# Kernel optimization log

Hardware: AMD Instinct MI355X
Metric: run time of the kernel (lower is better)

Reference implementation:

```python
import jax, jax.numpy as jnp
import numpy as np

ALPHA = 0.2  # LeakyReLU negative slope
NEG_INF = -9e15

def leaky_relu(x):
    return jnp.where(x >= 0, x, ALPHA * x)

def setup_inputs() -> dict:
    key = jax.random.key(0)
    ks = jax.random.split(key, 7)
    B, N, D = 8, 1024, 256
    R = 12
    return {
        "h0": jax.random.normal(ks[0], (B, N, D), jnp.float32),
        "h1": jax.random.normal(ks[1], (B, N, D), jnp.float32),
        "multi_adj": jax.random.randint(ks[2], (R, B, N, N), 0, 2, jnp.int32),
        "adj": jax.random.randint(ks[3], (B, N, N), 0, 2, jnp.int32),
        "W": jax.random.normal(ks[4], (D, D), jnp.float32) * 0.05,
        "a": jax.random.normal(ks[5], (2 * D,), jnp.float32) * 0.05,
        "A_rel": jax.random.normal(ks[6], (R, 2 * D), jnp.float32) * 0.05,
    }

def reference(h0, h1, multi_adj, adj, W, a, A_rel):
    D = W.shape[1]
    Wh0 = jnp.einsum('bnd,de->bne', h0, W)  # [B,N0,D]
    Wh1 = jnp.einsum('bnd,de->bne', h1, W)  # [B,N1,D]
    # a_input @ v decomposes into outer-sum of per-node projections
    s0 = Wh0 @ a[:D]                         # [B,N0]
    s1 = Wh1 @ a[D:]                         # [B,N1]
    e = leaky_relu(s0[:, :, None] + s1[:, None, :])  # [B,N0,N1]
    attention = jnp.where(adj > 0, e, NEG_INF)
    # 12 relation score maps, fused: r0[r,b,i] + r1[r,b,j]
    r0 = jnp.einsum('bnd,rd->rbn', Wh0, A_rel[:, :D])  # [R,B,N0]
    r1 = jnp.einsum('bnd,rd->rbn', Wh1, A_rel[:, D:])  # [R,B,N1]
    e_rel = leaky_relu(r0[:, :, :, None] + r1[:, :, None, :])  # [R,B,N0,N1]
    rel_sum = jnp.where(multi_adj > 0, e_rel, 0.0).sum(axis=0)  # [B,N0,N1]
    # note: original softmax is over dim=1 (source-node axis N0)
    att = jax.nn.softmax(attention + 0.01 * rel_sum, axis=1)
    # dropout omitted (eval mode / deterministic baseline)
    h_prime = jnp.einsum('bij,bjd->bid', att, Wh1)
    return jax.nn.elu(h_prime)  # concat=True
```

## Files before the change

### kernel.cpp

```cpp
#include <hip/hip_runtime.h>
#include <hip/hip_bf16.h>
#include <hip/hip_fp16.h>

#define BB 8
#define NN 1024
#define DD 256
#define RR 12
#define BN (BB * NN)
#define ICH 16
#define CCH (NN / ICH)

typedef __attribute__((ext_vector_type(8))) short short8v;
typedef __attribute__((ext_vector_type(4))) float f32x4;
typedef __attribute__((ext_vector_type(4))) int int4v;
typedef __attribute__((ext_vector_type(2))) uint uint2v;

static __device__ __forceinline__ ushort f2bf(float f) {
  union { float f; uint u; } v; v.f = f;
  uint r = v.u + 0x7FFF + ((v.u >> 16) & 1);
  return (ushort)(r >> 16);
}
static __device__ __forceinline__ uint pack2(float a, float b) {
  return (uint)f2bf(a) | ((uint)f2bf(b) << 16);
}
static __device__ __forceinline__ float bfround(float f) {
  union { uint u; float f; } v; v.u = (uint)f2bf(f) << 16;
  return v.f;
}

__global__ __launch_bounds__(256) void k_prep(const float* __restrict__ W,
                                              const float* __restrict__ a,
                                              const float* __restrict__ A_rel,
                                              ushort* __restrict__ WTb,
                                              float* __restrict__ Vt,
                                              float* __restrict__ lsum) {
  __shared__ float Ls[64][65];
  int blk = blockIdx.x, tid = threadIdx.x;
  if (blk < 16) {
    int k0 = (blk & 3) * 64, d0 = (blk >> 2) * 64;
    int rr = tid >> 4, c = (tid & 15) * 4;
#pragma unroll
    for (int p = 0; p < 4; ++p) {
      int row = p * 16 + rr;
      float4 v = *(const float4*)&W[(k0 + row) * DD + d0 + c];
      Ls[row][c] = v.x; Ls[row][c + 1] = v.y; Ls[row][c + 2] = v.z; Ls[row][c + 3] = v.w;
    }
    __syncthreads();
    int r2 = tid >> 3, cc = (tid & 7) * 8;
#pragma unroll
    for (int p = 0; p < 2; ++p) {
      int d = p * 32 + r2;
      uint4 q;
      q.x = pack2(Ls[cc + 0][d], Ls[cc + 1][d]);
      q.y = pack2(Ls[cc + 2][d], Ls[cc + 3][d]);
      q.z = pack2(Ls[cc + 4][d], Ls[cc + 5][d]);
      q.w = pack2(Ls[cc + 6][d], Ls[cc + 7][d]);
      *(uint4*)&WTb[(d0 + d) * DD + k0 + cc] = q;
    }
  } else if (blk == 68) {
    float4 z = make_float4(0.f, 0.f, 0.f, 0.f);
#pragma unroll
    for (int p = 0; p < 8; ++p)
      *(float4*)&lsum[(p * 256 + tid) * 4] = z;
  } else {
    int idx = blk - 16;
    int half = idx >= 26 ? 1 : 0;
    int c = idx - half * 26;
    if (c >= 13) return;
    int lane = tid & 63, w = tid >> 6;
    const float* X = (c == 0) ? &a[half * DD] : &A_rel[(c - 1) * 2 * DD + half * DD];
    float4 x4 = *(const float4*)&X[lane * 4];
    for (int kk = 0; kk < 64; ++kk) {
      int k = kk * 4 + w;
      float4 w4 = *(const float4*)&W[k * DD + lane * 4];
      float p = w4.x * x4.x + w4.y * x4.y + w4.z * x4.z + w4.w * x4.w;
#pragma unroll
      for (int off = 32; off; off >>= 1) p += __shfl_xor(p, off);
      if (lane == 0) Vt[(half * 13 + c) * DD + k] = p;
    }
  }
}

__global__ __launch_bounds__(256) void k_proj(const float* __restrict__ h0,
                                              const float* __restrict__ h1,
                                              const float* __restrict__ Vt,
                                              float* __restrict__ s0, float* __restrict__ s1,
                                              float* __restrict__ r0, float* __restrict__ r1) {
  int wid = (blockIdx.x * 256 + threadIdx.x) >> 6;
  int lane = threadIdx.x & 63;
  int mat = wid >> 13;
  int row = wid & (BN - 1);
  const float* h = mat ? h1 : h0;
  float4 h4 = *(const float4*)&h[(long)row * DD + lane * 4];
  float p[13];
#pragma unroll
  for (int c = 0; c < 13; ++c) {
    float4 v4 = *(const float4*)&Vt[(mat * 13 + c) * DD + lane * 4];
    p[c] = h4.x * v4.x + h4.y * v4.y + h4.z * v4.z + h4.w * v4.w;
  }
#pragma unroll
  for (int off = 32; off; off >>= 1)
#pragma unroll
    for (int c = 0; c < 13; ++c) p[c] += __shfl_xor(p[c], off);
  if (lane == 0) {
    if (mat == 0) {
      s0[row] = p[0];
      for (int c = 1; c < 13; ++c) r0[(c - 1) * BN + row] = p[c];
    } else {
      s1[row] = p[0];
      for (int c = 1; c < 13; ++c) r1[(c - 1) * BN + row] = p[c];
    }
  }
}

__global__ __launch_bounds__(256) void k_scores(const int* __restrict__ madj,
                                                const int* __restrict__ adj,
                                                const float* __restrict__ s0,
                                                const float* __restrict__ s1,
                                                const float* __restrict__ r0,
                                                const float* __restrict__ r1,
                                                ushort* __restrict__ U,
                                                float* __restrict__ lsum) {
  int b = blockIdx.x, c = blockIdx.y;
  int tid = threadIdx.x;
  int j4 = tid * 4;
  int i0 = c * ICH;
  __shared__ float s0c[ICH];
  __shared__ float r0c[RR][ICH];
  if (tid < (RR + 1) * ICH) {
    int v = tid / ICH, i = tid % ICH;
    float x = (v == 0) ? s0[b * NN + i0 + i] : r0[(v - 1) * BN + b * NN + i0 + i];
    if (v == 0) s0c[i] = x; else r0c[v - 1][i] = x;
  }
  __syncthreads();
  float4 s14 = *(const float4*)&s1[b * NN + j4];
  float rel[ICH][4] = {};
#pragma unroll 1
  for (int r = 0; r < RR; ++r) {
    float4 r1v = *(const float4*)&r1[r * BN + b * NN + j4];
    const int* mbase = &madj[(((long)r * BB + b) * NN + i0) * NN + j4];
#pragma unroll
    for (int i = 0; i < ICH; ++i) {
      int4v mv = __builtin_nontemporal_load((const int4v*)(mbase + (long)i * NN));
      float r0v = r0c[r][i];
      float t0 = r0v + r1v.x; t0 = fmaxf(t0, 0.2f * t0);
      float t1 = r0v + r1v.y; t1 = fmaxf(t1, 0.2f * t1);
      float t2 = r0v + r1v.z; t2 = fmaxf(t2, 0.2f * t2);
      float t3 = r0v + r1v.w; t3 = fmaxf(t3, 0.2f * t3);
      if (mv.x > 0) rel[i][0] += t0;
      if (mv.y > 0) rel[i][1] += t1;
      if (mv.z > 0) rel[i][2] += t2;
      if (mv.w > 0) rel[i][3] += t3;
    }
  }
  float l0 = 0.f, l1 = 0.f, l2 = 0.f, l3 = 0.f;
  const int* abase = &adj[((long)b * NN + i0) * NN + j4];
#pragma unroll
  for (int i = 0; i < ICH; ++i) {
    int4v av = __builtin_nontemporal_load((const int4v*)(abase + (long)i * NN));
    float s0v = s0c[i];
    float u0, u1, u2, u3;
    { float e = s0v + s14.x; e = fmaxf(e, 0.2f * e);
      u0 = __expf((av.x > 0 ? e : -9e15f) + 0.01f * rel[i][0] - 4.0f); }
    { float e = s0v + s14.y; e = fmaxf(e, 0.2f * e);
      u1 = __expf((av.y > 0 ? e : -9e15f) + 0.01f * rel[i][1] - 4.0f); }
    { float e = s0v + s14.z; e = fmaxf(e, 0.2f * e);
      u2 = __expf((av.z > 0 ? e : -9e15f) + 0.01f * rel[i][2] - 4.0f); }
    { float e = s0v + s14.w; e = fmaxf(e, 0.2f * e);
      u3 = __expf((av.w > 0 ? e : -9e15f) + 0.01f * rel[i][3] - 4.0f); }
    u0 = bfround(u0); u1 = bfround(u1); u2 = bfround(u2); u3 = bfround(u3);
    uint2v so;
    so.x = pack2(u0, u1);
    so.y = pack2(u2, u3);
    *(uint2v*)&U[((long)b * NN + i0 + i) * NN + j4] = so;
    l0 += u0; l1 += u1; l2 += u2; l3 += u3;
  }
  float* lp = &lsum[b * NN + j4];
  atomicAdd(lp + 0, l0);
  atomicAdd(lp + 1, l1);
  atomicAdd(lp + 2, l2);
  atomicAdd(lp + 3, l3);
}

__global__ __launch_bounds__(256) void k_mm_wh1(const float* __restrict__ h1,
                                                const ushort* __restrict__ WTb,
                                                const float* __restrict__ lsum,
                                                ushort* __restrict__ WhT) {
  __shared__ __align__(16) char smraw[24576];
  uint4* AswQ = (uint4*)smraw;
  uint4* BswQ = (uint4*)(smraw + 8192);
  typedef ushort LtRow[72];
  LtRow* Lt = (LtRow*)smraw;
  int n0 = blockIdx.x * 128, i0 = blockIdx.y * 64;
  int tid = threadIdx.x;
  int r = tid >> 3, cs = tid & 7;
  int lane = tid & 63, wid = tid >> 6;
  int wm = wid >> 1, wn = wid & 1;
  int lr = lane & 15, g = lane >> 4;
  f32x4 acc[2][4] = {};
  for (int k0 = 0; k0 < DD; k0 += 64) {
#pragma unroll
    for (int p = 0; p < 2; ++p) {
      int row = p * 32 + r;
      const float* src = h1 + (long)(i0 + row) * DD + k0 + cs * 8;
      float4 v0 = *(const float4*)src;
      float4 v1 = *(const float4*)(src + 4);
      uint4 q;
      q.x = pack2(v0.x, v0.y); q.y = pack2(v0.z, v0.w);
      q.z = pack2(v1.x, v1.y); q.w = pack2(v1.z, v1.w);
      AswQ[row * 8 + (cs ^ (row & 7))] = q;
    }
#pragma unroll
    for (int p = 0; p < 4; ++p) {
      int row = p * 32 + r;
      uint4 q = *(const uint4*)(WTb + (long)(n0 + row) * DD + k0 + cs * 8);
      BswQ[row * 8 + (cs ^ (row & 7))] = q;
    }
    __syncthreads();
#pragma unroll
    for (int ks = 0; ks < 2; ++ks) {
      short8v af[2], bfr[4];
      int slot = ks * 4 + g;
#pragma unroll
      for (int mi = 0; mi < 2; ++mi) {
        int row = wm * 32 + mi * 16 + lr;
        af[mi] = *reinterpret_cast<const short8v*>(&AswQ[row * 8 + (slot ^ (row & 7))]);
      }
#pragma unroll
      for (int ni = 0; ni < 4; ++ni) {
        int row = wn * 64 + ni * 16 + lr;
        bfr[ni] = *reinterpret_cast<const short8v*>(&BswQ[row * 8 + (slot ^ (row & 7))]);
      }
#pragma unroll
      for (int mi = 0; mi < 2; ++mi)
#pragma unroll
        for (int ni = 0; ni < 4; ++ni)
          acc[mi][ni] = __builtin_amdgcn_mfma_f32_16x16x32_bf16(af[mi], bfr[ni], acc[mi][ni], 0, 0, 0);
    }
    __syncthreads();
  }
#pragma unroll
  for (int mi = 0; mi < 2; ++mi) {
    int ib = wm * 32 + mi * 16 + g * 4;
    float4 lv = *(const float4*)&lsum[i0 + ib];
    float inv0 = 1.0f / lv.x, inv1 = 1.0f / lv.y, inv2 = 1.0f / lv.z, inv3 = 1.0f / lv.w;
#pragma unroll
    for (int ni = 0; ni < 4; ++ni) {
      int d = wn * 64 + ni * 16 + lr;
      uint2 w;
      w.x = pack2(acc[mi][ni][0] * inv0, acc[mi][ni][1] * inv1);
      w.y = pack2(acc[mi][ni][2] * inv2, acc[mi][ni][3] * inv3);
      *(uint2*)&Lt[d][ib] = w;
    }
  }
  __syncthreads();
  int b = i0 >> 10, il = i0 & 1023;
#pragma unroll
  for (int p = 0; p < 4; ++p) {
    int row = (tid >> 3) + p * 32;
    int ch = (tid & 7) * 8;
    uint4 q = *(uint4*)&Lt[row][ch];
    *(uint4*)&WhT[((long)b * DD + n0 + row) * NN + il + ch] = q;
  }
}

__global__ __launch_bounds__(256) void k_av(const ushort* __restrict__ U,
                                            const ushort* __restrict__ WhT,
                                            float* __restrict__ out) {
  __shared__ uint4 AswQ[64 * 8];
  __shared__ uint4 BswQ[64 * 8];
  int b = blockIdx.z;
  int i0 = blockIdx.y * 64;
  int n0 = blockIdx.x * 64;
  const ushort* Sb = U + (long)b * NN * NN;
  const ushort* Bb = WhT + (long)b * DD * NN;
  int tid = threadIdx.x;
  int r = tid >> 3, cs = tid & 7;
  int lane = tid & 63, wid = tid >> 6;
  int lr = lane & 15, g = lane >> 4;
  f32x4 acc[4] = {};
  for (int k0 = 0; k0 < NN; k0 += 64) {
#pragma unroll
    for (int p = 0; p < 2; ++p) {
      int row = p * 32 + r;
      AswQ[row * 8 + (cs ^ (row & 7))] =
          *(const uint4*)(Sb + (long)(i0 + row) * NN + k0 + cs * 8);
      BswQ[row * 8 + (cs ^ (row & 7))] =
          *(const uint4*)(Bb + (long)(n0 + row) * NN + k0 + cs * 8);
    }
    __syncthreads();
#pragma unroll
    for (int ks = 0; ks < 2; ++ks) {
      short8v af, bfr[4];
      int slot = ks * 4 + g;
      {
        int row = wid * 16 + lr;
        af = *reinterpret_cast<const short8v*>(&AswQ[row * 8 + (slot ^ (row & 7))]);
      }
#pragma unroll
      for (int ni = 0; ni < 4; ++ni) {
        int row = ni * 16 + lr;
        bfr[ni] = *reinterpret_cast<const short8v*>(&BswQ[row * 8 + (slot ^ (row & 7))]);
      }
#pragma unroll
      for (int ni = 0; ni < 4; ++ni)
        acc[ni] = __builtin_amdgcn_mfma_f32_16x16x32_bf16(af, bfr[ni], acc[ni], 0, 0, 0);
    }
    __syncthreads();
  }
#pragma unroll
  for (int ni = 0; ni < 4; ++ni)
#pragma unroll
    for (int q = 0; q < 4; ++q) {
      int row = i0 + wid * 16 + g * 4 + q;
      int col = n0 + ni * 16 + lr;
      float x = acc[ni][q];
      x = x > 0.f ? x : expm1f(x);
      out[((long)b * NN + row) * DD + col] = x;
    }
}

extern "C" void kernel_launch(void* const* d_in, const int* in_sizes, int n_in,
                              void* d_out, int out_size, void* d_ws, size_t ws_size,
                              hipStream_t stream) {
  const float* h0 = (const float*)d_in[0];
  const float* h1 = (const float*)d_in[1];
  const int* madj = (const int*)d_in[2];
  const int* adj = (const int*)d_in[3];
  const float* W = (const float*)d_in[4];
  const float* a = (const float*)d_in[5];
  const float* A_rel = (const float*)d_in[6];
  float* out = (float*)d_out;

  float* ws = (float*)d_ws;
  float* s0 = ws;
  float* s1 = s0 + BN;
  float* r0 = s1 + BN;
  float* r1 = r0 + RR * BN;
  float* lsum = r1 + RR * BN;
  float* Vt = lsum + BN;
  ushort* WTb = (ushort*)(Vt + 26 * DD);
  ushort* WhT = WTb + DD * DD;
  ushort* Uh = WhT + (size_t)BB * DD * NN;

  k_prep<<<69, 256, 0, stream>>>(W, a, A_rel, WTb, Vt, lsum);
  k_proj<<<(2 * BN) / 4, 256, 0, stream>>>(h0, h1, Vt, s0, s1, r0, r1);
  k_scores<<<dim3(BB, CCH), 256, 0, stream>>>(madj, adj, s0, s1, r0, r1, Uh, lsum);
  k_mm_wh1<<<dim3(2, BN / 64), 256, 0, stream>>>(h1, WTb, lsum, WhT);
  k_av<<<dim3(DD / 64, NN / 64, BB), 256, 0, stream>>>(Uh, WhT, out);
}
```

Measured before the change: 199.9 us.

## Split prep projections across more blocks, shrink score chunks, prefetch AV tiles

The Vt projection work in k_prep is now spread over 8 sub-blocks per vector, so 225 blocks run instead of a few long serial loops. k_scores halves the row chunk (ICH 16→8), doubling the block count, swaps the grid order so blocks sharing a batch launch together, and unrolls the relation loop by two. k_av register-prefetches the next K tile of U and WhT while the current tile is consumed, so global loads overlap the MFMA work. These changes raise parallelism and latency hiding in exchange for more blocks, more registers per thread and smaller per-block reuse of the s0/r0 values.

```diff
diff --git a/kernel.cpp b/kernel.cpp
--- a/kernel.cpp
+++ b/kernel.cpp
@@ -7,7 +7,7 @@
 #define DD 256
 #define RR 12
 #define BN (BB * NN)
-#define ICH 16
+#define ICH 8
 #define CCH (NN / ICH)
 
 typedef __attribute__((ext_vector_type(8))) short short8v;
@@ -57,21 +57,23 @@
       q.w = pack2(Ls[cc + 6][d], Ls[cc + 7][d]);
       *(uint4*)&WTb[(d0 + d) * DD + k0 + cc] = q;
     }
-  } else if (blk == 68) {
+  } else if (blk == 224) {
     float4 z = make_float4(0.f, 0.f, 0.f, 0.f);
 #pragma unroll
     for (int p = 0; p < 8; ++p)
       *(float4*)&lsum[(p * 256 + tid) * 4] = z;
   } else {
     int idx = blk - 16;
-    int half = idx >= 26 ? 1 : 0;
-    int c = idx - half * 26;
-    if (c >= 13) return;
+    int combo = idx >> 3;
+    int sub = idx & 7;
+    int half = combo >= 13 ? 1 : 0;
+    int c = combo - half * 13;
     int lane = tid & 63, w = tid >> 6;
     const float* X = (c == 0) ? &a[half * DD] : &A_rel[(c - 1) * 2 * DD + half * DD];
     float4 x4 = *(const float4*)&X[lane * 4];
-    for (int kk = 0; kk < 64; ++kk) {
-      int k = kk * 4 + w;
+#pragma unroll
+    for (int kk = 0; kk < 8; ++kk) {
+      int k = sub * 32 + kk * 4 + w;
       float4 w4 = *(const float4*)&W[k * DD + lane * 4];
       float p = w4.x * x4.x + w4.y * x4.y + w4.z * x4.z + w4.w * x4.w;
 #pragma unroll
@@ -121,7 +123,7 @@
                                                 const float* __restrict__ r1,
                                                 ushort* __restrict__ U,
                                                 float* __restrict__ lsum) {
-  int b = blockIdx.x, c = blockIdx.y;
+  int c = blockIdx.x, b = blockIdx.y;
   int tid = threadIdx.x;
   int j4 = tid * 4;
   int i0 = c * ICH;
@@ -135,13 +137,13 @@
   __syncthreads();
   float4 s14 = *(const float4*)&s1[b * NN + j4];
   float rel[ICH][4] = {};
-#pragma unroll 1
+#pragma unroll 2
   for (int r = 0; r < RR; ++r) {
     float4 r1v = *(const float4*)&r1[r * BN + b * NN + j4];
-    const int* mbase = &madj[(((long)r * BB + b) * NN + i0) * NN + j4];
 #pragma unroll
     for (int i = 0; i < ICH; ++i) {
-      int4v mv = __builtin_nontemporal_load((const int4v*)(mbase + (long)i * NN));
+      int4v mv = __builtin_nontemporal_load(
+          (const int4v*)&madj[(((long)r * BB + b) * NN + i0 + i) * NN + j4]);
       float r0v = r0c[r][i];
       float t0 = r0v + r1v.x; t0 = fmaxf(t0, 0.2f * t0);
       float t1 = r0v + r1v.y; t1 = fmaxf(t1, 0.2f * t1);
@@ -154,10 +156,10 @@
     }
   }
   float l0 = 0.f, l1 = 0.f, l2 = 0.f, l3 = 0.f;
-  const int* abase = &adj[((long)b * NN + i0) * NN + j4];
 #pragma unroll
   for (int i = 0; i < ICH; ++i) {
-    int4v av = __builtin_nontemporal_load((const int4v*)(abase + (long)i * NN));
+    int4v av = __builtin_nontemporal_load(
+        (const int4v*)&adj[((long)b * NN + i0 + i) * NN + j4]);
     float s0v = s0c[i];
     float u0, u1, u2, u3;
     { float e = s0v + s14.x; e = fmaxf(e, 0.2f * e);
@@ -279,16 +281,29 @@
   int lane = tid & 63, wid = tid >> 6;
   int lr = lane & 15, g = lane >> 4;
   f32x4 acc[4] = {};
+  uint4 a_pf[2], b_pf[2];
+#pragma unroll
+  for (int p = 0; p < 2; ++p) {
+    int row = p * 32 + r;
+    a_pf[p] = *(const uint4*)(Sb + (long)(i0 + row) * NN + cs * 8);
+    b_pf[p] = *(const uint4*)(Bb + (long)(n0 + row) * NN + cs * 8);
+  }
   for (int k0 = 0; k0 < NN; k0 += 64) {
 #pragma unroll
     for (int p = 0; p < 2; ++p) {
       int row = p * 32 + r;
-      AswQ[row * 8 + (cs ^ (row & 7))] =
-          *(const uint4*)(Sb + (long)(i0 + row) * NN + k0 + cs * 8);
-      BswQ[row * 8 + (cs ^ (row & 7))] =
-          *(const uint4*)(Bb + (long)(n0 + row) * NN + k0 + cs * 8);
-    }
-    __syncthreads();
+      AswQ[row * 8 + (cs ^ (row & 7))] = a_pf[p];
+      BswQ[row * 8 + (cs ^ (row & 7))] = b_pf[p];
+    }
+    __syncthreads();
+    if (k0 + 64 < NN) {
+#pragma unroll
+      for (int p = 0; p < 2; ++p) {
+        int row = p * 32 + r;
+        a_pf[p] = *(const uint4*)(Sb + (long)(i0 + row) * NN + k0 + 64 + cs * 8);
+        b_pf[p] = *(const uint4*)(Bb + (long)(n0 + row) * NN + k0 + 64 + cs * 8);
+      }
+    }
 #pragma unroll
     for (int ks = 0; ks < 2; ++ks) {
       short8v af, bfr[4];
@@ -343,9 +358,9 @@
   ushort* WhT = WTb + DD * DD;
   ushort* Uh = WhT + (size_t)BB * DD * NN;
 
-  k_prep<<<69, 256, 0, stream>>>(W, a, A_rel, WTb, Vt, lsum);
+  k_prep<<<225, 256, 0, stream>>>(W, a, A_rel, WTb, Vt, lsum);
   k_proj<<<(2 * BN) / 4, 256, 0, stream>>>(h0, h1, Vt, s0, s1, r0, r1);
-  k_scores<<<dim3(BB, CCH), 256, 0, stream>>>(madj, adj, s0, s1, r0, r1, Uh, lsum);
+  k_scores<<<dim3(CCH, BB), 256, 0, stream>>>(madj, adj, s0, s1, r0, r1, Uh, lsum);
   k_mm_wh1<<<dim3(2, BN / 64), 256, 0, stream>>>(h1, WTb, lsum, WhT);
   k_av<<<dim3(DD / 64, NN / 64, BB), 256, 0, stream>>>(Uh, WhT, out);
 }
```

Result: faster. 178.9 us (-10.5%).
